# Kernel optimization log

Measured on AMD Instinct MI355X. Metric: run time of the kernel, lower is better.

## Reference

```python
import jax, jax.numpy as jnp
import numpy as np

N, IN_DIM, OUT_DIM, HEADS = 8192, 256, 64, 2

def setup_inputs() -> dict:
    key = jax.random.key(0)
    k1, k2, k3, k4, k5 = jax.random.split(key, 5)
    x = jax.random.normal(k1, (N, IN_DIM), dtype=jnp.float32)
    adj = jax.random.randint(k2, (N, N), 0, 2, dtype=jnp.int32)
    # nn.Linear(in_dim, out_dim*heads, bias=False): weight [out_dim*heads, in_dim]
    W = jax.random.normal(k3, (OUT_DIM * HEADS, IN_DIM), dtype=jnp.float32) / np.sqrt(IN_DIM)
    attn_l = jax.random.normal(k4, (HEADS, OUT_DIM), dtype=jnp.float32)
    attn_r = jax.random.normal(k5, (HEADS, OUT_DIM), dtype=jnp.float32)
    return {"x": x, "adj": adj, "W": W, "attn_l": attn_l, "attn_r": attn_r}

def reference(x, adj, W, attn_l, attn_r):
    n = x.shape[0]
    h = (x @ W.T).reshape(n, HEADS, OUT_DIM)          # [N, H, D]
    el = jnp.einsum('nhd,hd->nh', h, attn_l)           # [N, H]
    er = jnp.einsum('nhd,hd->nh', h, attn_r)           # [N, H]
    e = el[:, None, :] + er[None, :, :]                # [N, N, H]
    e = jnp.where(adj[:, :, None] == 0, -jnp.inf, e)
    a = jax.nn.softmax(e, axis=1)                      # softmax over source nodes j
    out = jnp.einsum('ijh,jhd->ihd', a, h)             # [N, H, D]
    return out.reshape(n, HEADS * OUT_DIM)
```

## Files before the change

kernel.cpp:

```cpp
#include <hip/hip_runtime.h>
#include <cstdint>
#include <cstddef>

#define N_NODES 8192
#define IN_DIM  256
#define OUT_DIM 64
#define HEADS   2
#define FEAT    128
#define NTILES  9
#define ACC_STRIDE 132
#define KSPLIT  4

typedef __bf16 bf16x8 __attribute__((ext_vector_type(8)));
typedef float  f32x4  __attribute__((ext_vector_type(4)));

static __device__ __forceinline__ unsigned short f2bf(float f) {
  unsigned u = __float_as_uint(f);
  u += 0x7FFFu + ((u >> 16) & 1u);
  return (unsigned short)(u >> 16);
}

__global__ void k_vr(const float* __restrict__ W, const float* __restrict__ attn_r,
                     float* __restrict__ vr) {
  const int t = threadIdx.x;
  const int h = t >> 8, k = t & 255;
  float s = 0.f;
  for (int d = 0; d < OUT_DIM; d++)
    s += attn_r[h*OUT_DIM + d] * W[(size_t)(h*OUT_DIM + d)*IN_DIM + k];
  vr[h*IN_DIM + k] = s;
}

__global__ __launch_bounds__(256) void k_h(const float* __restrict__ x,
                                           const float* __restrict__ W,
                                           float* __restrict__ H) {
  const int rb = blockIdx.x >> 1, cb = blockIdx.x & 1;
  __shared__ float xs[32][68];
  __shared__ float wl[32][68];
  const int tid = threadIdx.x;
  const int ty = tid >> 4, tx = tid & 15;
  float acc[4][4] = {};
  for (int kc = 0; kc < IN_DIM; kc += 32) {
    __syncthreads();
    {
      const int r = tid >> 3, kk = (tid & 7) * 4;
      float4 xv = *(const float4*)(x + (size_t)(rb*64 + r)*IN_DIM + kc + kk);
      xs[kk+0][r] = xv.x; xs[kk+1][r] = xv.y; xs[kk+2][r] = xv.z; xs[kk+3][r] = xv.w;
      float4 xv2 = *(const float4*)(x + (size_t)(rb*64 + r + 32)*IN_DIM + kc + kk);
      xs[kk+0][r+32] = xv2.x; xs[kk+1][r+32] = xv2.y; xs[kk+2][r+32] = xv2.z; xs[kk+3][r+32] = xv2.w;
      float4 wv = *(const float4*)(W + (size_t)(cb*64 + r)*IN_DIM + kc + kk);
      wl[kk+0][r] = wv.x; wl[kk+1][r] = wv.y; wl[kk+2][r] = wv.z; wl[kk+3][r] = wv.w;
      float4 wv2 = *(const float4*)(W + (size_t)(cb*64 + r + 32)*IN_DIM + kc + kk);
      wl[kk+0][r+32] = wv2.x; wl[kk+1][r+32] = wv2.y; wl[kk+2][r+32] = wv2.z; wl[kk+3][r+32] = wv2.w;
    }
    __syncthreads();
#pragma unroll
    for (int k = 0; k < 32; k++) {
      float xr[4], wr[4];
#pragma unroll
      for (int i = 0; i < 4; i++) { xr[i] = xs[k][ty + i*16]; wr[i] = wl[k][tx + i*16]; }
#pragma unroll
      for (int i = 0; i < 4; i++)
#pragma unroll
        for (int j = 0; j < 4; j++) acc[i][j] = fmaf(xr[i], wr[j], acc[i][j]);
    }
  }
#pragma unroll
  for (int i = 0; i < 4; i++)
#pragma unroll
    for (int j = 0; j < 4; j++)
      H[(size_t)(rb*64 + ty + i*16)*FEAT + cb*64 + tx + j*16] = acc[i][j];
}

__global__ void k_er(const float* __restrict__ x, const float* __restrict__ vr,
                     float* __restrict__ er) {
  const int wave = threadIdx.x >> 6, lane = threadIdx.x & 63;
  const int j = blockIdx.x*4 + wave;
  float4 xv = ((const float4*)(x + (size_t)j*IN_DIM))[lane];
  float4 a0 = ((const float4*)vr)[lane];
  float4 a1 = ((const float4*)(vr + IN_DIM))[lane];
  float s0 = xv.x*a0.x + xv.y*a0.y + xv.z*a0.z + xv.w*a0.w;
  float s1 = xv.x*a1.x + xv.y*a1.y + xv.z*a1.z + xv.w*a1.w;
#pragma unroll
  for (int off = 32; off > 0; off >>= 1) {
    s0 += __shfl_down(s0, off);
    s1 += __shfl_down(s1, off);
  }
  if (lane == 0) { er[j*2+0] = s0; er[j*2+1] = s1; }
}

__global__ void k_pack(const float* __restrict__ H, const float* __restrict__ er,
                       unsigned short* __restrict__ frag) {
  const int oct = blockIdx.x;
  const int c = threadIdx.x;
  if (c >= 144) return;
  const int j0 = oct * 8;
  const int kb = oct >> 2, sub = oct & 3;
  unsigned short v[8];
  if (c < FEAT) {
    const int h = c >> 6;
#pragma unroll
    for (int t = 0; t < 8; t++) {
      float w = __expf(er[(j0 + t)*2 + h]);
      v[t] = f2bf(w * H[(size_t)(j0 + t)*FEAT + c]);
    }
  } else if (c < FEAT + HEADS) {
    const int h = c - FEAT;
#pragma unroll
    for (int t = 0; t < 8; t++) v[t] = f2bf(__expf(er[(j0 + t)*2 + h]));
  } else {
#pragma unroll
    for (int t = 0; t < 8; t++) v[t] = 0;
  }
  uint4 o;
  o.x = (unsigned)v[0] | ((unsigned)v[1] << 16);
  o.y = (unsigned)v[2] | ((unsigned)v[3] << 16);
  o.z = (unsigned)v[4] | ((unsigned)v[5] << 16);
  o.w = (unsigned)v[6] | ((unsigned)v[7] << 16);
  uint4* dst = (uint4*)frag + ((size_t)(kb*NTILES + (c >> 4)))*64 + (sub*16 + (c & 15));
  *dst = o;
}

__global__ void k_zero(float* __restrict__ p) {
  const int total = N_NODES * ACC_STRIDE / 4;
  for (int i = blockIdx.x*blockDim.x + threadIdx.x; i < total; i += gridDim.x*blockDim.x)
    ((float4*)p)[i] = (float4){0.f, 0.f, 0.f, 0.f};
}

__global__ __launch_bounds__(256, 2) void k_main(const int* __restrict__ adj,
                                                 const uint4* __restrict__ fragB,
                                                 float* __restrict__ accum) {
  const int bx = blockIdx.x;
  const int mb = bx >> 2;
  const int ks = bx & 3;
  const int tid = threadIdx.x;
  const int wave = tid >> 6, lane = tid & 63;
  const int m16 = lane & 15, quad = lane >> 4;
  const int rowA = mb*64 + wave*16 + m16;

  __shared__ uint4 ldsB[2][36*64];

  f32x4 dacc[NTILES];
#pragma unroll
  for (int n = 0; n < NTILES; n++) dacc[n] = (f32x4){0.f, 0.f, 0.f, 0.f};

  const int* abase = adj + (size_t)rowA*N_NODES + ks*2048 + quad*8;

  auto stageB = [&](int c, int buf) {
    const uint4* src = fragB + ((size_t)(ks*64 + c*4 + wave) * NTILES) * 64 + lane;
    uint4* dst = &ldsB[buf][(wave*NTILES)*64 + lane];
#pragma unroll
    for (int t = 0; t < NTILES; t++)
      __builtin_amdgcn_global_load_lds(
          (__attribute__((address_space(1))) void*)(src + t*64),
          (__attribute__((address_space(3))) void*)(dst + t*64), 16, 0, 0);
  };

  auto prefA = [&](int c, int4 (&A)[8]) {
#pragma unroll
    for (int kl = 0; kl < 4; kl++) {
      const int* p = abase + (c*4 + kl)*32;
      A[kl*2+0] = *(const int4*)(p);
      A[kl*2+1] = *(const int4*)(p + 4);
    }
  };

  auto compute = [&](int buf, int4 (&A)[8]) {
    const uint4* lb = &ldsB[buf][0];
#pragma unroll
    for (int kl = 0; kl < 4; kl++) {
      const int* ai = (const int*)(&A[kl*2]);
      unsigned u0 = (ai[0] ? 0x3F80u : 0u) | (ai[1] ? 0x3F800000u : 0u);
      unsigned u1 = (ai[2] ? 0x3F80u : 0u) | (ai[3] ? 0x3F800000u : 0u);
      unsigned u2 = (ai[4] ? 0x3F80u : 0u) | (ai[5] ? 0x3F800000u : 0u);
      unsigned u3 = (ai[6] ? 0x3F80u : 0u) | (ai[7] ? 0x3F800000u : 0u);
      bf16x8 af = __builtin_bit_cast(bf16x8, make_uint4(u0, u1, u2, u3));
#pragma unroll
      for (int n = 0; n < NTILES; n++) {
        bf16x8 bfr = __builtin_bit_cast(bf16x8, lb[(kl*NTILES + n)*64 + lane]);
        dacc[n] = __builtin_amdgcn_mfma_f32_16x16x32_bf16(af, bfr, dacc[n], 0, 0, 0);
      }
    }
  };

  int4 A0[8], A1[8];
  prefA(0, A0);
  stageB(0, 0);
#pragma unroll
  for (int cc = 0; cc < 8; cc++) {
    __syncthreads();
    stageB(2*cc + 1, 1);
    prefA(2*cc + 1, A1);
    compute(0, A0);
    __syncthreads();
    if (cc < 7) { stageB(2*cc + 2, 0); prefA(2*cc + 2, A0); }
    compute(1, A1);
  }

  const int rb = mb*64 + wave*16 + quad*4;
#pragma unroll
  for (int n = 0; n < NTILES; n++) {
    if (n == 8 && m16 >= HEADS) continue;
#pragma unroll
    for (int r = 0; r < 4; r++)
      atomicAdd(&accum[(size_t)(rb + r)*ACC_STRIDE + n*16 + m16], dacc[n][r]);
  }
}

__global__ void k_div(const float* __restrict__ acc, float* __restrict__ out) {
  const int i = blockIdx.x, c = threadIdx.x;
  const float d = acc[(size_t)i*ACC_STRIDE + FEAT + (c >> 6)];
  out[(size_t)i*FEAT + c] = acc[(size_t)i*ACC_STRIDE + c] / d;
}

extern "C" void kernel_launch(void* const* d_in, const int* in_sizes, int n_in,
                              void* d_out, int out_size, void* d_ws, size_t ws_size,
                              hipStream_t stream) {
  const float* x      = (const float*)d_in[0];
  const int*   adj    = (const int*)  d_in[1];
  const float* W      = (const float*)d_in[2];
  const float* attn_r = (const float*)d_in[4];

  char* ws = (char*)d_ws;
  float* vr            = (float*)(ws + 0);
  float* er            = (float*)(ws + 4096);
  float* H             = (float*)(ws + 131072);
  unsigned short* frag = (unsigned short*)(ws + 4325376);
  float* acc           = (float*)(ws + 6684672);
  float* out           = (float*)d_out;

  hipLaunchKernelGGL(k_vr,   dim3(1),    dim3(512), 0, stream, W, attn_r, vr);
  hipLaunchKernelGGL(k_h,    dim3(256),  dim3(256), 0, stream, x, W, H);
  hipLaunchKernelGGL(k_er,   dim3(2048), dim3(256), 0, stream, x, vr, er);
  hipLaunchKernelGGL(k_pack, dim3(1024), dim3(192), 0, stream, H, er, frag);
  hipLaunchKernelGGL(k_zero, dim3(512),  dim3(256), 0, stream, acc);
  hipLaunchKernelGGL(k_main, dim3(512),  dim3(256), 0, stream, adj, (const uint4*)frag, acc);
  hipLaunchKernelGGL(k_div,  dim3(8192), dim3(128), 0, stream, acc, out);
}
```

Measured before the change: 436.0 us.

## Restructure main GEMM: 32-row waves, register-staged B, split-K partials without atomics

The main adjacency-times-features kernel now gives each wave 32 rows, two 16-row MFMA tiles that share one B fragment. B is loaded straight into registers with double buffering, replacing the LDS staging and block barriers, and adj is read with nontemporal loads. Split-K goes from 4 to 8 slices, each writing its own partial buffer instead of using atomics, so the zero kernel is dropped and k_div sums the eight partials. The input projection kernel also switches to row-major LDS tiles with float4 reads and a K step of 64. The trade-off is more register pressure, duplicate global B reads per wave, and a larger partial buffer to read back in k_div.

```diff
diff --git a/kernel.cpp b/kernel.cpp
--- a/kernel.cpp
+++ b/kernel.cpp
@@ -9,10 +9,12 @@
 #define FEAT    128
 #define NTILES  9
 #define ACC_STRIDE 132
-#define KSPLIT  4
+#define KSPLIT  8
 
 typedef __bf16 bf16x8 __attribute__((ext_vector_type(8)));
 typedef float  f32x4  __attribute__((ext_vector_type(4)));
+typedef int    i32x4  __attribute__((ext_vector_type(4)));
+typedef unsigned uu32x4 __attribute__((ext_vector_type(4)));
 
 static __device__ __forceinline__ unsigned short f2bf(float f) {
   unsigned u = __float_as_uint(f);
@@ -34,34 +36,34 @@
                                            const float* __restrict__ W,
                                            float* __restrict__ H) {
   const int rb = blockIdx.x >> 1, cb = blockIdx.x & 1;
-  __shared__ float xs[32][68];
-  __shared__ float wl[32][68];
+  __shared__ float xs[64][68];
+  __shared__ float wl[64][68];
   const int tid = threadIdx.x;
   const int ty = tid >> 4, tx = tid & 15;
   float acc[4][4] = {};
-  for (int kc = 0; kc < IN_DIM; kc += 32) {
+  for (int kc = 0; kc < IN_DIM; kc += 64) {
     __syncthreads();
-    {
-      const int r = tid >> 3, kk = (tid & 7) * 4;
-      float4 xv = *(const float4*)(x + (size_t)(rb*64 + r)*IN_DIM + kc + kk);
-      xs[kk+0][r] = xv.x; xs[kk+1][r] = xv.y; xs[kk+2][r] = xv.z; xs[kk+3][r] = xv.w;
-      float4 xv2 = *(const float4*)(x + (size_t)(rb*64 + r + 32)*IN_DIM + kc + kk);
-      xs[kk+0][r+32] = xv2.x; xs[kk+1][r+32] = xv2.y; xs[kk+2][r+32] = xv2.z; xs[kk+3][r+32] = xv2.w;
-      float4 wv = *(const float4*)(W + (size_t)(cb*64 + r)*IN_DIM + kc + kk);
-      wl[kk+0][r] = wv.x; wl[kk+1][r] = wv.y; wl[kk+2][r] = wv.z; wl[kk+3][r] = wv.w;
-      float4 wv2 = *(const float4*)(W + (size_t)(cb*64 + r + 32)*IN_DIM + kc + kk);
-      wl[kk+0][r+32] = wv2.x; wl[kk+1][r+32] = wv2.y; wl[kk+2][r+32] = wv2.z; wl[kk+3][r+32] = wv2.w;
+#pragma unroll
+    for (int p = 0; p < 4; p++) {
+      const int idx = p*256 + tid;
+      const int r = idx >> 4, k4 = idx & 15;
+      *(float4*)&xs[r][k4*4] = *(const float4*)(x + (size_t)(rb*64 + r)*IN_DIM + kc + k4*4);
+      *(float4*)&wl[r][k4*4] = *(const float4*)(W + (size_t)(cb*64 + r)*IN_DIM + kc + k4*4);
     }
     __syncthreads();
 #pragma unroll
-    for (int k = 0; k < 32; k++) {
-      float xr[4], wr[4];
-#pragma unroll
-      for (int i = 0; i < 4; i++) { xr[i] = xs[k][ty + i*16]; wr[i] = wl[k][tx + i*16]; }
+    for (int k4 = 0; k4 < 16; k4++) {
+      float4 xr[4], wr[4];
+#pragma unroll
+      for (int i = 0; i < 4; i++) {
+        xr[i] = *(const float4*)&xs[ty + i*16][k4*4];
+        wr[i] = *(const float4*)&wl[tx + i*16][k4*4];
+      }
 #pragma unroll
       for (int i = 0; i < 4; i++)
 #pragma unroll
-        for (int j = 0; j < 4; j++) acc[i][j] = fmaf(xr[i], wr[j], acc[i][j]);
+        for (int j = 0; j < 4; j++)
+          acc[i][j] += xr[i].x*wr[j].x + xr[i].y*wr[j].y + xr[i].z*wr[j].z + xr[i].w*wr[j].w;
     }
   }
 #pragma unroll
@@ -120,96 +122,101 @@
   *dst = o;
 }
 
-__global__ void k_zero(float* __restrict__ p) {
-  const int total = N_NODES * ACC_STRIDE / 4;
-  for (int i = blockIdx.x*blockDim.x + threadIdx.x; i < total; i += gridDim.x*blockDim.x)
-    ((float4*)p)[i] = (float4){0.f, 0.f, 0.f, 0.f};
-}
-
 __global__ __launch_bounds__(256, 2) void k_main(const int* __restrict__ adj,
                                                  const uint4* __restrict__ fragB,
                                                  float* __restrict__ accum) {
-  const int bx = blockIdx.x;
-  const int mb = bx >> 2;
-  const int ks = bx & 3;
+  const int mb = blockIdx.x >> 3;
+  const int ks = blockIdx.x & 7;
   const int tid = threadIdx.x;
   const int wave = tid >> 6, lane = tid & 63;
   const int m16 = lane & 15, quad = lane >> 4;
-  const int rowA = mb*64 + wave*16 + m16;
-
-  __shared__ uint4 ldsB[2][36*64];
-
-  f32x4 dacc[NTILES];
-#pragma unroll
-  for (int n = 0; n < NTILES; n++) dacc[n] = (f32x4){0.f, 0.f, 0.f, 0.f};
-
-  const int* abase = adj + (size_t)rowA*N_NODES + ks*2048 + quad*8;
-
-  auto stageB = [&](int c, int buf) {
-    const uint4* src = fragB + ((size_t)(ks*64 + c*4 + wave) * NTILES) * 64 + lane;
-    uint4* dst = &ldsB[buf][(wave*NTILES)*64 + lane];
+
+  const int row0 = mb*128 + wave*32 + m16;
+  const int* a0 = adj + (size_t)row0*N_NODES + ks*1024 + quad*8;
+  const int* a1 = a0 + (size_t)16*N_NODES;
+  const uint4* bb = fragB + (size_t)(ks*32)*NTILES*64 + lane;
+
+  f32x4 acc0[NTILES], acc1[NTILES];
+#pragma unroll
+  for (int n = 0; n < NTILES; n++) {
+    acc0[n] = (f32x4){0.f, 0.f, 0.f, 0.f};
+    acc1[n] = (f32x4){0.f, 0.f, 0.f, 0.f};
+  }
+
+  i32x4  Abuf[2][4];
+  uu32x4 Bbuf[2][NTILES];
+
+  auto loadA = [&](int kk, int buf) {
+    const i32x4* p0 = (const i32x4*)(a0 + kk*32);
+    const i32x4* p1 = (const i32x4*)(a1 + kk*32);
+    Abuf[buf][0] = __builtin_nontemporal_load(p0);
+    Abuf[buf][1] = __builtin_nontemporal_load(p0 + 1);
+    Abuf[buf][2] = __builtin_nontemporal_load(p1);
+    Abuf[buf][3] = __builtin_nontemporal_load(p1 + 1);
+  };
+  auto loadB = [&](int kk, int buf) {
+    const uu32x4* b = (const uu32x4*)bb;
 #pragma unroll
     for (int t = 0; t < NTILES; t++)
-      __builtin_amdgcn_global_load_lds(
-          (__attribute__((address_space(1))) void*)(src + t*64),
-          (__attribute__((address_space(3))) void*)(dst + t*64), 16, 0, 0);
-  };
-
-  auto prefA = [&](int c, int4 (&A)[8]) {
-#pragma unroll
-    for (int kl = 0; kl < 4; kl++) {
-      const int* p = abase + (c*4 + kl)*32;
-      A[kl*2+0] = *(const int4*)(p);
-      A[kl*2+1] = *(const int4*)(p + 4);
-    }
-  };
-
-  auto compute = [&](int buf, int4 (&A)[8]) {
-    const uint4* lb = &ldsB[buf][0];
-#pragma unroll
-    for (int kl = 0; kl < 4; kl++) {
-      const int* ai = (const int*)(&A[kl*2]);
-      unsigned u0 = (ai[0] ? 0x3F80u : 0u) | (ai[1] ? 0x3F800000u : 0u);
-      unsigned u1 = (ai[2] ? 0x3F80u : 0u) | (ai[3] ? 0x3F800000u : 0u);
-      unsigned u2 = (ai[4] ? 0x3F80u : 0u) | (ai[5] ? 0x3F800000u : 0u);
-      unsigned u3 = (ai[6] ? 0x3F80u : 0u) | (ai[7] ? 0x3F800000u : 0u);
-      bf16x8 af = __builtin_bit_cast(bf16x8, make_uint4(u0, u1, u2, u3));
-#pragma unroll
-      for (int n = 0; n < NTILES; n++) {
-        bf16x8 bfr = __builtin_bit_cast(bf16x8, lb[(kl*NTILES + n)*64 + lane]);
-        dacc[n] = __builtin_amdgcn_mfma_f32_16x16x32_bf16(af, bfr, dacc[n], 0, 0, 0);
-      }
-    }
-  };
-
-  int4 A0[8], A1[8];
-  prefA(0, A0);
-  stageB(0, 0);
-#pragma unroll
-  for (int cc = 0; cc < 8; cc++) {
-    __syncthreads();
-    stageB(2*cc + 1, 1);
-    prefA(2*cc + 1, A1);
-    compute(0, A0);
-    __syncthreads();
-    if (cc < 7) { stageB(2*cc + 2, 0); prefA(2*cc + 2, A0); }
-    compute(1, A1);
-  }
-
-  const int rb = mb*64 + wave*16 + quad*4;
+      Bbuf[buf][t] = b[(size_t)(kk*NTILES + t)*64];
+  };
+  auto conv = [&](const i32x4* A) -> bf16x8 {
+    const int* ai = (const int*)A;
+    unsigned u0 = (ai[0] ? 0x3F80u : 0u) | (ai[1] ? 0x3F800000u : 0u);
+    unsigned u1 = (ai[2] ? 0x3F80u : 0u) | (ai[3] ? 0x3F800000u : 0u);
+    unsigned u2 = (ai[4] ? 0x3F80u : 0u) | (ai[5] ? 0x3F800000u : 0u);
+    unsigned u3 = (ai[6] ? 0x3F80u : 0u) | (ai[7] ? 0x3F800000u : 0u);
+    uu32x4 u = {u0, u1, u2, u3};
+    return __builtin_bit_cast(bf16x8, u);
+  };
+  auto compute = [&](int buf) {
+    bf16x8 af0 = conv(&Abuf[buf][0]);
+    bf16x8 af1 = conv(&Abuf[buf][2]);
+#pragma unroll
+    for (int n = 0; n < NTILES; n++) {
+      bf16x8 bfr = __builtin_bit_cast(bf16x8, Bbuf[buf][n]);
+      acc0[n] = __builtin_amdgcn_mfma_f32_16x16x32_bf16(af0, bfr, acc0[n], 0, 0, 0);
+    }
+#pragma unroll
+    for (int n = 0; n < NTILES; n++) {
+      bf16x8 bfr = __builtin_bit_cast(bf16x8, Bbuf[buf][n]);
+      acc1[n] = __builtin_amdgcn_mfma_f32_16x16x32_bf16(af1, bfr, acc1[n], 0, 0, 0);
+    }
+  };
+
+  loadA(0, 0); loadB(0, 0);
+  for (int kk = 0; kk < 32; kk += 2) {
+    loadA(kk + 1, 1); loadB(kk + 1, 1);
+    compute(0);
+    const int k2 = (kk + 2 < 32) ? kk + 2 : 31;
+    loadA(k2, 0); loadB(k2, 0);
+    compute(1);
+  }
+
+  const int rb0 = mb*128 + wave*32 + quad*4;
+  float* op = accum + (size_t)ks*N_NODES*ACC_STRIDE;
 #pragma unroll
   for (int n = 0; n < NTILES; n++) {
     if (n == 8 && m16 >= HEADS) continue;
 #pragma unroll
-    for (int r = 0; r < 4; r++)
-      atomicAdd(&accum[(size_t)(rb + r)*ACC_STRIDE + n*16 + m16], dacc[n][r]);
+    for (int r = 0; r < 4; r++) {
+      op[(size_t)(rb0 + r)*ACC_STRIDE + n*16 + m16]      = acc0[n][r];
+      op[(size_t)(rb0 + 16 + r)*ACC_STRIDE + n*16 + m16] = acc1[n][r];
+    }
   }
 }
 
 __global__ void k_div(const float* __restrict__ acc, float* __restrict__ out) {
   const int i = blockIdx.x, c = threadIdx.x;
-  const float d = acc[(size_t)i*ACC_STRIDE + FEAT + (c >> 6)];
-  out[(size_t)i*FEAT + c] = acc[(size_t)i*ACC_STRIDE + c] / d;
+  const int h = c >> 6;
+  float num = 0.f, den = 0.f;
+#pragma unroll
+  for (int s = 0; s < KSPLIT; s++) {
+    const float* p = acc + ((size_t)s*N_NODES + i)*ACC_STRIDE;
+    num += p[c];
+    den += p[FEAT + h];
+  }
+  out[(size_t)i*FEAT + c] = num / den;
 }
 
 extern "C" void kernel_launch(void* const* d_in, const int* in_sizes, int n_in,
@@ -232,7 +239,6 @@
   hipLaunchKernelGGL(k_h,    dim3(256),  dim3(256), 0, stream, x, W, H);
   hipLaunchKernelGGL(k_er,   dim3(2048), dim3(256), 0, stream, x, vr, er);
   hipLaunchKernelGGL(k_pack, dim3(1024), dim3(192), 0, stream, H, er, frag);
-  hipLaunchKernelGGL(k_zero, dim3(512),  dim3(256), 0, stream, acc);
   hipLaunchKernelGGL(k_main, dim3(512),  dim3(256), 0, stream, adj, (const uint4*)frag, acc);
   hipLaunchKernelGGL(k_div,  dim3(8192), dim3(128), 0, stream, acc, out);
 }
```

New measurement: 440.8 us. About the same (+1.1%).
